# Kernel optimization log

Hardware: AMD Instinct MI355X
Metric: run time of the kernel (lower is better)

Reference implementation:

```python
import jax, jax.numpy as jnp
import numpy as np

N_NODES = 100000
N_EDGES = 1000000
NODE_DIM = 64
HIDDEN_DIM = 128


def setup_inputs() -> dict:
    key = jax.random.key(0)
    ks = jax.random.split(key, 9)
    x = jax.random.normal(ks[0], (N_NODES, NODE_DIM), dtype=jnp.float32)
    y = jax.random.normal(ks[1], (N_NODES, NODE_DIM), dtype=jnp.float32)
    edge_index = jax.random.randint(ks[2], (2, N_EDGES), 0, N_NODES, dtype=jnp.int64)
    pos_x = jax.random.normal(ks[3], (N_NODES, 3), dtype=jnp.float32)
    pos_y = jax.random.normal(ks[4], (N_NODES, 3), dtype=jnp.float32)
    in_dim = NODE_DIM * 2 + 1
    # Kaiming-uniform-ish init like torch Linear
    lim1 = 1.0 / np.sqrt(in_dim)
    lim2 = 1.0 / np.sqrt(HIDDEN_DIM)
    W1 = jax.random.uniform(ks[5], (in_dim, HIDDEN_DIM), jnp.float32, -lim1, lim1)
    b1 = jax.random.uniform(ks[6], (HIDDEN_DIM,), jnp.float32, -lim1, lim1)
    W2 = jax.random.uniform(ks[7], (HIDDEN_DIM, 1), jnp.float32, -lim2, lim2)
    b2 = jax.random.uniform(ks[8], (1,), jnp.float32, -lim2, lim2)
    return {"x": x, "y": y, "edge_index": edge_index, "pos_x": pos_x,
            "pos_y": pos_y, "W1": W1, "b1": b1, "W2": W2, "b2": b2}


def reference(x, y, edge_index, pos_x, pos_y, W1, b1, W2, b2):
    src = edge_index[0]
    dst = edge_index[1]
    # per-edge euclidean distance between endpoint positions  [E]
    d = pos_x[src] - pos_y[dst]                      # [E, 3]
    dist = jnp.sqrt(jnp.sum(d * d, axis=1))          # [E]
    # gather + concat: [E, node_dim*2 + 1]
    mlp_in = jnp.concatenate([x[src], y[dst], dist[:, None]], axis=1)
    h = jax.nn.relu(mlp_in @ W1 + b1)                # [E, hidden]
    out = jax.nn.relu(h @ W2 + b2)                   # [E, 1]
    return out
```

## Files before the change

kernel.cpp:

```cpp
#include <hip/hip_runtime.h>
#include <hip/hip_bf16.h>


constexpr int NDIM  = 64;
constexpr int HID   = 128;
constexpr int KPAD  = 136;

typedef __attribute__((ext_vector_type(8))) short  short8;
typedef __attribute__((ext_vector_type(4))) int    int4v;
typedef __attribute__((ext_vector_type(4))) float  floatx4;

__device__ __forceinline__ short f2bf(float f) {
    union { __hip_bfloat16 h; short s; } cv;
    cv.h = __float2bfloat16(f);
    return cv.s;
}

__device__ __forceinline__ int pack2(float a, float b) {
    union { __hip_bfloat162 h; int u; } cv;
    cv.h = __float22bfloat162_rn(float2{a, b});
    return cv.u;
}

__device__ __forceinline__ short8 make_afrag_f32(const float* rp) {
    const floatx4 f0 = *reinterpret_cast<const floatx4*>(rp);
    const floatx4 f1 = *reinterpret_cast<const floatx4*>(rp + 4);
    union { int4v i; short8 s8; } cv;
    cv.i.x = pack2(f0.x, f0.y);
    cv.i.y = pack2(f0.z, f0.w);
    cv.i.z = pack2(f1.x, f1.y);
    cv.i.w = pack2(f1.z, f1.w);
    return cv.s8;
}

__device__ __forceinline__ float bf2f(short s) {
    union { __hip_bfloat16 h; short v; } cv;
    cv.v = s;
    return __bfloat162float(cv.h);
}

__global__ __launch_bounds__(256) void cvt_kernel(
    const float* __restrict__ xin, const float* __restrict__ yin,
    short* __restrict__ xb, short* __restrict__ yb, int nfl)
{
    const int stride = gridDim.x * blockDim.x;
    const int n8 = nfl >> 3;
    for (int i = blockIdx.x * blockDim.x + threadIdx.x; i < n8; i += stride) {
        {
            const floatx4 f0 = *reinterpret_cast<const floatx4*>(xin + i * 8);
            const floatx4 f1 = *reinterpret_cast<const floatx4*>(xin + i * 8 + 4);
            union { int4v v; short8 s; } c;
            c.v.x = pack2(f0.x, f0.y); c.v.y = pack2(f0.z, f0.w);
            c.v.z = pack2(f1.x, f1.y); c.v.w = pack2(f1.z, f1.w);
            *reinterpret_cast<short8*>(xb + i * 8) = c.s;
        }
        {
            const floatx4 f0 = *reinterpret_cast<const floatx4*>(yin + i * 8);
            const floatx4 f1 = *reinterpret_cast<const floatx4*>(yin + i * 8 + 4);
            union { int4v v; short8 s; } c;
            c.v.x = pack2(f0.x, f0.y); c.v.y = pack2(f0.z, f0.w);
            c.v.z = pack2(f1.x, f1.y); c.v.w = pack2(f1.z, f1.w);
            *reinterpret_cast<short8*>(yb + i * 8) = c.s;
        }
    }
}

template <bool BF16GATHER>
__global__ __launch_bounds__(256, 2) void edge_mlp_kernel(
    const float* __restrict__ x, const float* __restrict__ y,
    const short* __restrict__ xb, const short* __restrict__ yb,
    const int*  __restrict__ ei, const float* __restrict__ px,
    const float* __restrict__ py, const float* __restrict__ W1,
    const float* __restrict__ b1, const float* __restrict__ W2,
    const float* __restrict__ b2, float* __restrict__ out, int E)
{
    __shared__ __align__(16) short Wt[HID * KPAD];
    const int tid = threadIdx.x;

    for (int base = 0; base < HID * HID; base += 256 * 8) {
        float f[8];
#pragma unroll
        for (int u = 0; u < 8; ++u) f[u] = W1[base + u * 256 + tid];
#pragma unroll
        for (int u = 0; u < 8; ++u) {
            int i = base + u * 256 + tid;
            Wt[(i & 127) * KPAD + (i >> 7)] = f2bf(f[u]);
        }
    }
    __syncthreads();

    const int lane = tid & 63;
    const int wave = tid >> 6;
    const int quad = lane >> 4;
    const int lm   = lane & 15;

    float w2v[8], w1rv[8], b1v[8];
#pragma unroll
    for (int t = 0; t < 8; ++t) {
        const int n = t * 16 + lm;
        w2v[t]  = W2[n];
        w1rv[t] = bf2f(f2bf(W1[128 * HID + n]));
        b1v[t]  = bf2f(f2bf(b1[n]));
    }
    const float b2s = b2[0];

    const int* __restrict__ srcp = ei;
    const int* __restrict__ dstp = ei + E;

    const short* wr = Wt + lm * KPAD + quad * 8;
    short8 wg[6][4];
#pragma unroll
    for (int t = 0; t < 6; ++t)
#pragma unroll
        for (int c = 0; c < 4; ++c)
            wg[t][c] = *reinterpret_cast<const short8*>(wr + t * (16 * KPAD) + c * 32);

    const int ntiles = (E + 127) / 128;
    for (int tile = blockIdx.x; tile < ntiles; tile += gridDim.x) {
        const int mb = tile * 128 + wave * 32;
        int m0 = mb + lm;       if (m0 >= E) m0 = E - 1;
        int m1 = mb + 16 + lm;  if (m1 >= E) m1 = E - 1;
        const int src0 = srcp[m0], dst0 = dstp[m0];
        const int src1 = srcp[m1], dst1 = dstp[m1];

        float dd = 0.f;
        if (lane < 32) {
            const int ps = (lane < 16) ? src0 : src1;
            const int pd = (lane < 16) ? dst0 : dst1;
            const float ax = px[ps * 3 + 0] - py[pd * 3 + 0];
            const float ay = px[ps * 3 + 1] - py[pd * 3 + 1];
            const float az = px[ps * 3 + 2] - py[pd * 3 + 2];
            dd = sqrtf(ax * ax + ay * ay + az * az);
        }
        float dfA[4], dfB[4];
#pragma unroll
        for (int r = 0; r < 4; ++r) {
            const float dA = __shfl(dd, quad * 4 + r, 64);
            const float dB = __shfl(dd, 16 + quad * 4 + r, 64);
            dfA[r] = bf2f(f2bf(dA));
            dfB[r] = bf2f(f2bf(dB));
        }

        short8 fa[4], fb[4];
#pragma unroll
        for (int c = 0; c < 4; ++c) {
            const int kk = c * 32 + quad * 8;
            if (BF16GATHER) {
                const short* pa = (c < 2) ? (xb + src0 * NDIM + kk)
                                          : (yb + dst0 * NDIM + (kk - 64));
                const short* pb = (c < 2) ? (xb + src1 * NDIM + kk)
                                          : (yb + dst1 * NDIM + (kk - 64));
                fa[c] = *reinterpret_cast<const short8*>(pa);
                fb[c] = *reinterpret_cast<const short8*>(pb);
            } else {
                fa[c] = make_afrag_f32((c < 2) ? (x + src0 * NDIM + kk)
                                               : (y + dst0 * NDIM + (kk - 64)));
                fb[c] = make_afrag_f32((c < 2) ? (x + src1 * NDIM + kk)
                                               : (y + dst1 * NDIM + (kk - 64)));
            }
        }

        float p0 = 0.f, p1 = 0.f, p2 = 0.f, p3 = 0.f;
        float q0 = 0.f, q1 = 0.f, q2 = 0.f, q3 = 0.f;

        int zoff = 0;
        asm volatile("" : "+v"(zoff));
        const short* wrs = Wt + zoff + lm * KPAD + quad * 8;

#pragma unroll
        for (int half = 0; half < 2; ++half) {
            if (half) __builtin_amdgcn_sched_barrier(0);

            floatx4 aA[4], aB[4];
#pragma unroll
            for (int u = 0; u < 4; ++u) {
                const int t = half * 4 + u;
                const float bi = b1v[t];
                aA[u] = floatx4{bi, bi, bi, bi};
                aB[u] = floatx4{bi, bi, bi, bi};
            }
#pragma unroll
            for (int u = 0; u < 4; ++u) {
                const int t = half * 4 + u;
                short8 bg0, bg1, bg2, bg3;
                if (t < 6) {
                    bg0 = wg[t][0]; bg1 = wg[t][1]; bg2 = wg[t][2]; bg3 = wg[t][3];
                } else {
                    const short* bp = wrs + t * (16 * KPAD);
                    bg0 = *reinterpret_cast<const short8*>(bp);
                    bg1 = *reinterpret_cast<const short8*>(bp + 32);
                    bg2 = *reinterpret_cast<const short8*>(bp + 64);
                    bg3 = *reinterpret_cast<const short8*>(bp + 96);
                }
                aA[u] = __builtin_amdgcn_mfma_f32_16x16x32_bf16(fa[0], bg0, aA[u], 0, 0, 0);
                aB[u] = __builtin_amdgcn_mfma_f32_16x16x32_bf16(fb[0], bg0, aB[u], 0, 0, 0);
                aA[u] = __builtin_amdgcn_mfma_f32_16x16x32_bf16(fa[1], bg1, aA[u], 0, 0, 0);
                aB[u] = __builtin_amdgcn_mfma_f32_16x16x32_bf16(fb[1], bg1, aB[u], 0, 0, 0);
                aA[u] = __builtin_amdgcn_mfma_f32_16x16x32_bf16(fa[2], bg2, aA[u], 0, 0, 0);
                aB[u] = __builtin_amdgcn_mfma_f32_16x16x32_bf16(fb[2], bg2, aB[u], 0, 0, 0);
                aA[u] = __builtin_amdgcn_mfma_f32_16x16x32_bf16(fa[3], bg3, aA[u], 0, 0, 0);
                aB[u] = __builtin_amdgcn_mfma_f32_16x16x32_bf16(fb[3], bg3, aB[u], 0, 0, 0);
            }
#pragma unroll
            for (int u = 0; u < 4; ++u) {
                const int t = half * 4 + u;
                const float w  = w2v[t];
                const float wr1 = w1rv[t];
                p0 += fmaxf(fmaf(dfA[0], wr1, aA[u][0]), 0.f) * w;
                p1 += fmaxf(fmaf(dfA[1], wr1, aA[u][1]), 0.f) * w;
                p2 += fmaxf(fmaf(dfA[2], wr1, aA[u][2]), 0.f) * w;
                p3 += fmaxf(fmaf(dfA[3], wr1, aA[u][3]), 0.f) * w;
                q0 += fmaxf(fmaf(dfB[0], wr1, aB[u][0]), 0.f) * w;
                q1 += fmaxf(fmaf(dfB[1], wr1, aB[u][1]), 0.f) * w;
                q2 += fmaxf(fmaf(dfB[2], wr1, aB[u][2]), 0.f) * w;
                q3 += fmaxf(fmaf(dfB[3], wr1, aB[u][3]), 0.f) * w;
            }
        }

#pragma unroll
        for (int off = 1; off < 16; off <<= 1) {
            p0 += __shfl_xor(p0, off, 64);
            p1 += __shfl_xor(p1, off, 64);
            p2 += __shfl_xor(p2, off, 64);
            p3 += __shfl_xor(p3, off, 64);
            q0 += __shfl_xor(q0, off, 64);
            q1 += __shfl_xor(q1, off, 64);
            q2 += __shfl_xor(q2, off, 64);
            q3 += __shfl_xor(q3, off, 64);
        }
        if (lm < 4) {
            const float vA = (lm == 0) ? p0 : (lm == 1) ? p1 : (lm == 2) ? p2 : p3;
            const float vB = (lm == 0) ? q0 : (lm == 1) ? q1 : (lm == 2) ? q2 : q3;
            const int eA = mb + quad * 4 + lm;
            const int eB = mb + 16 + quad * 4 + lm;
            if (eA < E) out[eA] = fmaxf(vA + b2s, 0.f);
            if (eB < E) out[eB] = fmaxf(vB + b2s, 0.f);
        }
    }
}

extern "C" void kernel_launch(void* const* d_in, const int* in_sizes, int n_in,
                              void* d_out, int out_size, void* d_ws, size_t ws_size,
                              hipStream_t stream)
{
    const float* x  = (const float*)d_in[0];
    const float* y  = (const float*)d_in[1];
    const int*   ei = (const int*)  d_in[2];
    const float* px = (const float*)d_in[3];
    const float* py = (const float*)d_in[4];
    const float* W1 = (const float*)d_in[5];
    const float* b1 = (const float*)d_in[6];
    const float* W2 = (const float*)d_in[7];
    const float* b2 = (const float*)d_in[8];
    float* out = (float*)d_out;
    const int E = in_sizes[2] / 2;
    const int nnode_elems = in_sizes[0];

    const size_t need = (size_t)nnode_elems * 2 * sizeof(short);
    if (ws_size >= need) {
        short* xb = (short*)d_ws;
        short* yb = xb + nnode_elems;
        cvt_kernel<<<dim3(1024), dim3(256), 0, stream>>>(x, y, xb, yb, nnode_elems);
        edge_mlp_kernel<true><<<dim3(1024), dim3(256), 0, stream>>>(
            x, y, xb, yb, ei, px, py, W1, b1, W2, b2, out, E);
    } else {
        edge_mlp_kernel<false><<<dim3(1024), dim3(256), 0, stream>>>(
            x, y, nullptr, nullptr, ei, px, py, W1, b1, W2, b2, out, E);
    }
}
```

Baseline: 166.3 us.

## Software-pipeline gathers across tiles with double-buffered fragments and higher occupancy

Restructures the persistent tile loop into a two-stage software pipeline: edge indices are prefetched two tiles ahead and the gathered x/y bf16 fragments for the next tile are loaded while the current tile's MFMAs run. Position loads are issued early and the distance math is deferred until after the first MFMA half. To free registers for the double buffers, the W1 fragments are no longer cached in registers and are read from LDS every tile. Launch bounds go from 2 to 3 blocks per SM and the grid from 1024 to 768 blocks. The aim is to hide random-gather latency, at the cost of more LDS traffic and register pressure that could cause spills.

Measured after the change: 218.0 us. +31.1%, slower.

```diff
diff --git a/kernel.cpp b/kernel.cpp
--- a/kernel.cpp
+++ b/kernel.cpp
@@ -65,8 +65,151 @@
     }
 }
 
+struct IdxB { int s0, d0, s1, d1; };
+
+__device__ __forceinline__ void load_idx(int tile, int wave, int lm, int E,
+    const int* __restrict__ srcp, const int* __restrict__ dstp, IdxB& I)
+{
+    const int mb = tile * 128 + wave * 32;
+    int m0 = mb + lm;       if (m0 >= E) m0 = E - 1;
+    int m1 = mb + 16 + lm;  if (m1 >= E) m1 = E - 1;
+    I.s0 = srcp[m0]; I.d0 = dstp[m0];
+    I.s1 = srcp[m1]; I.d1 = dstp[m1];
+}
+
+struct FragB { short8 fa[4]; short8 fb[4]; };
+
 template <bool BF16GATHER>
-__global__ __launch_bounds__(256, 2) void edge_mlp_kernel(
+__device__ __forceinline__ void load_frags(const IdxB& I,
+    const float* __restrict__ x, const float* __restrict__ y,
+    const short* __restrict__ xb, const short* __restrict__ yb,
+    int quad, FragB& F)
+{
+#pragma unroll
+    for (int c = 0; c < 4; ++c) {
+        const int kk = c * 32 + quad * 8;
+        if (BF16GATHER) {
+            const short* pa = (c < 2) ? (xb + I.s0 * NDIM + kk)
+                                      : (yb + I.d0 * NDIM + (kk - 64));
+            const short* pb = (c < 2) ? (xb + I.s1 * NDIM + kk)
+                                      : (yb + I.d1 * NDIM + (kk - 64));
+            F.fa[c] = *reinterpret_cast<const short8*>(pa);
+            F.fb[c] = *reinterpret_cast<const short8*>(pb);
+        } else {
+            F.fa[c] = make_afrag_f32((c < 2) ? (x + I.s0 * NDIM + kk)
+                                             : (y + I.d0 * NDIM + (kk - 64)));
+            F.fb[c] = make_afrag_f32((c < 2) ? (x + I.s1 * NDIM + kk)
+                                             : (y + I.d1 * NDIM + (kk - 64)));
+        }
+    }
+}
+
+__device__ __forceinline__ void compute_tile(
+    const IdxB& I, const FragB& F, int tile, int E,
+    const short* __restrict__ Wt,
+    const float* __restrict__ px, const float* __restrict__ py,
+    int lane, int lm, int quad, int wave,
+    const float* w2v, const float* w1rv, const float* b1v, float b2s,
+    float* __restrict__ out)
+{
+    float pa0 = 0.f, pa1 = 0.f, pa2 = 0.f, pb0 = 0.f, pb1 = 0.f, pb2 = 0.f;
+    if (lane < 32) {
+        const int ps = (lane < 16) ? I.s0 : I.s1;
+        const int pd = (lane < 16) ? I.d0 : I.d1;
+        pa0 = px[ps * 3 + 0]; pa1 = px[ps * 3 + 1]; pa2 = px[ps * 3 + 2];
+        pb0 = py[pd * 3 + 0]; pb1 = py[pd * 3 + 1]; pb2 = py[pd * 3 + 2];
+    }
+
+    float p0 = 0.f, p1 = 0.f, p2 = 0.f, p3 = 0.f;
+    float q0 = 0.f, q1 = 0.f, q2 = 0.f, q3 = 0.f;
+    float dfA[4], dfB[4];
+
+    int zoff = 0;
+    asm volatile("" : "+v"(zoff));
+    const short* wr = Wt + zoff + lm * KPAD + quad * 8;
+
+#pragma unroll
+    for (int half = 0; half < 2; ++half) {
+        if (half) __builtin_amdgcn_sched_barrier(0);
+
+        floatx4 aA[4], aB[4];
+#pragma unroll
+        for (int u = 0; u < 4; ++u) {
+            const float bi = b1v[half * 4 + u];
+            aA[u] = floatx4{bi, bi, bi, bi};
+            aB[u] = floatx4{bi, bi, bi, bi};
+        }
+#pragma unroll
+        for (int u = 0; u < 4; ++u) {
+            const int t = half * 4 + u;
+            const short* bp = wr + t * (16 * KPAD);
+            const short8 bg0 = *reinterpret_cast<const short8*>(bp);
+            const short8 bg1 = *reinterpret_cast<const short8*>(bp + 32);
+            const short8 bg2 = *reinterpret_cast<const short8*>(bp + 64);
+            const short8 bg3 = *reinterpret_cast<const short8*>(bp + 96);
+            aA[u] = __builtin_amdgcn_mfma_f32_16x16x32_bf16(F.fa[0], bg0, aA[u], 0, 0, 0);
+            aB[u] = __builtin_amdgcn_mfma_f32_16x16x32_bf16(F.fb[0], bg0, aB[u], 0, 0, 0);
+            aA[u] = __builtin_amdgcn_mfma_f32_16x16x32_bf16(F.fa[1], bg1, aA[u], 0, 0, 0);
+            aB[u] = __builtin_amdgcn_mfma_f32_16x16x32_bf16(F.fb[1], bg1, aB[u], 0, 0, 0);
+            aA[u] = __builtin_amdgcn_mfma_f32_16x16x32_bf16(F.fa[2], bg2, aA[u], 0, 0, 0);
+            aB[u] = __builtin_amdgcn_mfma_f32_16x16x32_bf16(F.fb[2], bg2, aB[u], 0, 0, 0);
+            aA[u] = __builtin_amdgcn_mfma_f32_16x16x32_bf16(F.fa[3], bg3, aA[u], 0, 0, 0);
+            aB[u] = __builtin_amdgcn_mfma_f32_16x16x32_bf16(F.fb[3], bg3, aB[u], 0, 0, 0);
+        }
+        if (half == 0) {
+            float dd = 0.f;
+            if (lane < 32) {
+                const float ax = pa0 - pb0;
+                const float ay = pa1 - pb1;
+                const float az = pa2 - pb2;
+                dd = sqrtf(ax * ax + ay * ay + az * az);
+            }
+#pragma unroll
+            for (int r = 0; r < 4; ++r) {
+                dfA[r] = bf2f(f2bf(__shfl(dd, quad * 4 + r, 64)));
+                dfB[r] = bf2f(f2bf(__shfl(dd, 16 + quad * 4 + r, 64)));
+            }
+        }
+#pragma unroll
+        for (int u = 0; u < 4; ++u) {
+            const int t = half * 4 + u;
+            const float w   = w2v[t];
+            const float wr1 = w1rv[t];
+            p0 += fmaxf(fmaf(dfA[0], wr1, aA[u][0]), 0.f) * w;
+            p1 += fmaxf(fmaf(dfA[1], wr1, aA[u][1]), 0.f) * w;
+            p2 += fmaxf(fmaf(dfA[2], wr1, aA[u][2]), 0.f) * w;
+            p3 += fmaxf(fmaf(dfA[3], wr1, aA[u][3]), 0.f) * w;
+            q0 += fmaxf(fmaf(dfB[0], wr1, aB[u][0]), 0.f) * w;
+            q1 += fmaxf(fmaf(dfB[1], wr1, aB[u][1]), 0.f) * w;
+            q2 += fmaxf(fmaf(dfB[2], wr1, aB[u][2]), 0.f) * w;
+            q3 += fmaxf(fmaf(dfB[3], wr1, aB[u][3]), 0.f) * w;
+        }
+    }
+
+#pragma unroll
+    for (int off = 1; off < 16; off <<= 1) {
+        p0 += __shfl_xor(p0, off, 64);
+        p1 += __shfl_xor(p1, off, 64);
+        p2 += __shfl_xor(p2, off, 64);
+        p3 += __shfl_xor(p3, off, 64);
+        q0 += __shfl_xor(q0, off, 64);
+        q1 += __shfl_xor(q1, off, 64);
+        q2 += __shfl_xor(q2, off, 64);
+        q3 += __shfl_xor(q3, off, 64);
+    }
+    if (lm < 4) {
+        const int mb = tile * 128 + wave * 32;
+        const float vA = (lm == 0) ? p0 : (lm == 1) ? p1 : (lm == 2) ? p2 : p3;
+        const float vB = (lm == 0) ? q0 : (lm == 1) ? q1 : (lm == 2) ? q2 : q3;
+        const int eA = mb + quad * 4 + lm;
+        const int eB = mb + 16 + quad * 4 + lm;
+        if (eA < E) out[eA] = fmaxf(vA + b2s, 0.f);
+        if (eB < E) out[eB] = fmaxf(vB + b2s, 0.f);
+    }
+}
+
+template <bool BF16GATHER>
+__global__ __launch_bounds__(256, 3) void edge_mlp_kernel(
     const float* __restrict__ x, const float* __restrict__ y,
     const short* __restrict__ xb, const short* __restrict__ yb,
     const int*  __restrict__ ei, const float* __restrict__ px,
@@ -107,135 +250,37 @@
     const int* __restrict__ srcp = ei;
     const int* __restrict__ dstp = ei + E;
 
-    const short* wr = Wt + lm * KPAD + quad * 8;
-    short8 wg[6][4];
-#pragma unroll
-    for (int t = 0; t < 6; ++t)
-#pragma unroll
-        for (int c = 0; c < 4; ++c)
-            wg[t][c] = *reinterpret_cast<const short8*>(wr + t * (16 * KPAD) + c * 32);
-
     const int ntiles = (E + 127) / 128;
-    for (int tile = blockIdx.x; tile < ntiles; tile += gridDim.x) {
-        const int mb = tile * 128 + wave * 32;
-        int m0 = mb + lm;       if (m0 >= E) m0 = E - 1;
-        int m1 = mb + 16 + lm;  if (m1 >= E) m1 = E - 1;
-        const int src0 = srcp[m0], dst0 = dstp[m0];
-        const int src1 = srcp[m1], dst1 = dstp[m1];
-
-        float dd = 0.f;
-        if (lane < 32) {
-            const int ps = (lane < 16) ? src0 : src1;
-            const int pd = (lane < 16) ? dst0 : dst1;
-            const float ax = px[ps * 3 + 0] - py[pd * 3 + 0];
-            const float ay = px[ps * 3 + 1] - py[pd * 3 + 1];
-            const float az = px[ps * 3 + 2] - py[pd * 3 + 2];
-            dd = sqrtf(ax * ax + ay * ay + az * az);
-        }
-        float dfA[4], dfB[4];
-#pragma unroll
-        for (int r = 0; r < 4; ++r) {
-            const float dA = __shfl(dd, quad * 4 + r, 64);
-            const float dB = __shfl(dd, 16 + quad * 4 + r, 64);
-            dfA[r] = bf2f(f2bf(dA));
-            dfB[r] = bf2f(f2bf(dB));
-        }
-
-        short8 fa[4], fb[4];
-#pragma unroll
-        for (int c = 0; c < 4; ++c) {
-            const int kk = c * 32 + quad * 8;
-            if (BF16GATHER) {
-                const short* pa = (c < 2) ? (xb + src0 * NDIM + kk)
-                                          : (yb + dst0 * NDIM + (kk - 64));
-                const short* pb = (c < 2) ? (xb + src1 * NDIM + kk)
-                                          : (yb + dst1 * NDIM + (kk - 64));
-                fa[c] = *reinterpret_cast<const short8*>(pa);
-                fb[c] = *reinterpret_cast<const short8*>(pb);
-            } else {
-                fa[c] = make_afrag_f32((c < 2) ? (x + src0 * NDIM + kk)
-                                               : (y + dst0 * NDIM + (kk - 64)));
-                fb[c] = make_afrag_f32((c < 2) ? (x + src1 * NDIM + kk)
-                                               : (y + dst1 * NDIM + (kk - 64)));
-            }
-        }
-
-        float p0 = 0.f, p1 = 0.f, p2 = 0.f, p3 = 0.f;
-        float q0 = 0.f, q1 = 0.f, q2 = 0.f, q3 = 0.f;
-
-        int zoff = 0;
-        asm volatile("" : "+v"(zoff));
-        const short* wrs = Wt + zoff + lm * KPAD + quad * 8;
-
-#pragma unroll
-        for (int half = 0; half < 2; ++half) {
-            if (half) __builtin_amdgcn_sched_barrier(0);
-
-            floatx4 aA[4], aB[4];
-#pragma unroll
-            for (int u = 0; u < 4; ++u) {
-                const int t = half * 4 + u;
-                const float bi = b1v[t];
-                aA[u] = floatx4{bi, bi, bi, bi};
-                aB[u] = floatx4{bi, bi, bi, bi};
-            }
-#pragma unroll
-            for (int u = 0; u < 4; ++u) {
-                const int t = half * 4 + u;
-                short8 bg0, bg1, bg2, bg3;
-                if (t < 6) {
-                    bg0 = wg[t][0]; bg1 = wg[t][1]; bg2 = wg[t][2]; bg3 = wg[t][3];
-                } else {
-                    const short* bp = wrs + t * (16 * KPAD);
-                    bg0 = *reinterpret_cast<const short8*>(bp);
-                    bg1 = *reinterpret_cast<const short8*>(bp + 32);
-                    bg2 = *reinterpret_cast<const short8*>(bp + 64);
-                    bg3 = *reinterpret_cast<const short8*>(bp + 96);
-                }
-                aA[u] = __builtin_amdgcn_mfma_f32_16x16x32_bf16(fa[0], bg0, aA[u], 0, 0, 0);
-                aB[u] = __builtin_amdgcn_mfma_f32_16x16x32_bf16(fb[0], bg0, aB[u], 0, 0, 0);
-                aA[u] = __builtin_amdgcn_mfma_f32_16x16x32_bf16(fa[1], bg1, aA[u], 0, 0, 0);
-                aB[u] = __builtin_amdgcn_mfma_f32_16x16x32_bf16(fb[1], bg1, aB[u], 0, 0, 0);
-                aA[u] = __builtin_amdgcn_mfma_f32_16x16x32_bf16(fa[2], bg2, aA[u], 0, 0, 0);
-                aB[u] = __builtin_amdgcn_mfma_f32_16x16x32_bf16(fb[2], bg2, aB[u], 0, 0, 0);
-                aA[u] = __builtin_amdgcn_mfma_f32_16x16x32_bf16(fa[3], bg3, aA[u], 0, 0, 0);
-                aB[u] = __builtin_amdgcn_mfma_f32_16x16x32_bf16(fb[3], bg3, aB[u], 0, 0, 0);
-            }
-#pragma unroll
-            for (int u = 0; u < 4; ++u) {
-                const int t = half * 4 + u;
-                const float w  = w2v[t];
-                const float wr1 = w1rv[t];
-                p0 += fmaxf(fmaf(dfA[0], wr1, aA[u][0]), 0.f) * w;
-                p1 += fmaxf(fmaf(dfA[1], wr1, aA[u][1]), 0.f) * w;
-                p2 += fmaxf(fmaf(dfA[2], wr1, aA[u][2]), 0.f) * w;
-                p3 += fmaxf(fmaf(dfA[3], wr1, aA[u][3]), 0.f) * w;
-                q0 += fmaxf(fmaf(dfB[0], wr1, aB[u][0]), 0.f) * w;
-                q1 += fmaxf(fmaf(dfB[1], wr1, aB[u][1]), 0.f) * w;
-                q2 += fmaxf(fmaf(dfB[2], wr1, aB[u][2]), 0.f) * w;
-                q3 += fmaxf(fmaf(dfB[3], wr1, aB[u][3]), 0.f) * w;
-            }
-        }
-
-#pragma unroll
-        for (int off = 1; off < 16; off <<= 1) {
-            p0 += __shfl_xor(p0, off, 64);
-            p1 += __shfl_xor(p1, off, 64);
-            p2 += __shfl_xor(p2, off, 64);
-            p3 += __shfl_xor(p3, off, 64);
-            q0 += __shfl_xor(q0, off, 64);
-            q1 += __shfl_xor(q1, off, 64);
-            q2 += __shfl_xor(q2, off, 64);
-            q3 += __shfl_xor(q3, off, 64);
-        }
-        if (lm < 4) {
-            const float vA = (lm == 0) ? p0 : (lm == 1) ? p1 : (lm == 2) ? p2 : p3;
-            const float vB = (lm == 0) ? q0 : (lm == 1) ? q1 : (lm == 2) ? q2 : q3;
-            const int eA = mb + quad * 4 + lm;
-            const int eB = mb + 16 + quad * 4 + lm;
-            if (eA < E) out[eA] = fmaxf(vA + b2s, 0.f);
-            if (eB < E) out[eB] = fmaxf(vB + b2s, 0.f);
-        }
+    const int step = gridDim.x;
+    int tile = blockIdx.x;
+    if (tile >= ntiles) return;
+
+    IdxB Ic, In; FragB Fa, Fb;
+    load_idx(tile, wave, lm, E, srcp, dstp, Ic);
+    load_idx(tile + step, wave, lm, E, srcp, dstp, In);
+    load_frags<BF16GATHER>(Ic, x, y, xb, yb, quad, Fa);
+
+#pragma unroll 1
+    for (;;) {
+        load_frags<BF16GATHER>(In, x, y, xb, yb, quad, Fb);
+        {
+            IdxB tmp = Ic;
+            load_idx(tile + 2 * step, wave, lm, E, srcp, dstp, Ic);
+            compute_tile(tmp, Fa, tile, E, Wt, px, py, lane, lm, quad, wave,
+                         w2v, w1rv, b1v, b2s, out);
+        }
+        tile += step;
+        if (tile >= ntiles) break;
+
+        load_frags<BF16GATHER>(Ic, x, y, xb, yb, quad, Fa);
+        {
+            IdxB tmp = In;
+            load_idx(tile + 2 * step, wave, lm, E, srcp, dstp, In);
+            compute_tile(tmp, Fb, tile, E, Wt, px, py, lane, lm, quad, wave,
+                         w2v, w1rv, b1v, b2s, out);
+        }
+        tile += step;
+        if (tile >= ntiles) break;
     }
 }
 
@@ -261,10 +306,10 @@
         short* xb = (short*)d_ws;
         short* yb = xb + nnode_elems;
         cvt_kernel<<<dim3(1024), dim3(256), 0, stream>>>(x, y, xb, yb, nnode_elems);
-        edge_mlp_kernel<true><<<dim3(1024), dim3(256), 0, stream>>>(
+        edge_mlp_kernel<true><<<dim3(768), dim3(256), 0, stream>>>(
             x, y, xb, yb, ei, px, py, W1, b1, W2, b2, out, E);
     } else {
-        edge_mlp_kernel<false><<<dim3(1024), dim3(256), 0, stream>>>(
+        edge_mlp_kernel<false><<<dim3(768), dim3(256), 0, stream>>>(
             x, y, nullptr, nullptr, ei, px, py, W1, b1, W2, b2, out, E);
     }
 }
```
